# Performance work log

Hardware: AMD Instinct MI355X
Metric: run time of the kernel (lower is better)

The kernel has to match this reference:

```python
import math
import jax, jax.numpy as jnp
import numpy as np

SIN_DIM = 8
HEADS = 4
HID = 64
EMBED = 6 + 1 + 3 * SIN_DIM + 5 + 2  # 38


def _sinusoidal(v):
    # v: [N] -> [N, SIN_DIM], interleaved sin/cos as in torch.stack(...).flatten(-2)
    div = jnp.exp(jnp.arange(0, SIN_DIM, 2, dtype=jnp.float32) * (-math.log(10000.0) / SIN_DIM))
    scaled = v[:, None] * div  # [N, SIN_DIM//2]
    return jnp.stack([jnp.sin(scaled), jnp.cos(scaled)], axis=-1).reshape(v.shape[0], SIN_DIM)


def _feature_embed(x):
    nt = jnp.clip(x[:, 0].astype(jnp.int32), 0, 5)
    role = jnp.clip(x[:, 5].astype(jnp.int32), 0, 4)
    return jnp.concatenate([
        jax.nn.one_hot(nt, 6, dtype=x.dtype),
        jnp.log1p(x[:, 1])[:, None],
        _sinusoidal(x[:, 2]),
        _sinusoidal(x[:, 3]),
        _sinusoidal(x[:, 4] * 100.0),
        jax.nn.one_hot(role, 5, dtype=x.dtype),
        x[:, 6:7],
        x[:, 7:8],
    ], axis=-1)  # [N, 38]


def _gat(x, adj, W, a_src, a_dst, concat):
    N = x.shape[0]
    h = (x @ W).reshape(N, HEADS, HID)                       # [N,H,D]
    src = jnp.einsum('nhd,hd->nh', h, a_src)                 # [N,H]
    dst = jnp.einsum('nhd,hd->nh', h, a_dst)                 # [N,H]
    e = src[:, None, :] + dst[None, :, :]                    # [N,N,H]
    e = jnp.where(e > 0, e, 0.2 * e)                         # leaky_relu(0.2)
    e = jnp.where(adj[:, :, None] > 0, e, -jnp.inf)
    a = jax.nn.softmax(e, axis=1)                            # softmax over neighbors j
    out = jnp.einsum('njh,nhd->nhd'.replace('nj', 'ij').replace('nhd,', 'jhd,').replace('->nhd', '->ihd'), a, h) if False else jnp.einsum('ijh,jhd->ihd', a, h)
    if concat:
        return out.reshape(N, HEADS * HID)
    return out.mean(axis=1)


def _layernorm(x, g, b, eps=1e-5):
    mu = x.mean(axis=-1, keepdims=True)
    var = ((x - mu) ** 2).mean(axis=-1, keepdims=True)
    return (x - mu) / jnp.sqrt(var + eps) * g + b


def setup_inputs() -> dict:
    key = jax.random.key(0)
    ks = jax.random.split(key, 16)
    N, C = 4096, 512
    # raw node features per FeatureEmbedding docstring
    nt = jax.random.randint(ks[0], (N,), 0, 6).astype(jnp.float32)
    arity = jax.random.randint(ks[1], (N,), 0, 5).astype(jnp.float32)
    arg_pos = jax.random.randint(ks[2], (N,), 0, 8).astype(jnp.float32)
    depth = jax.random.randint(ks[3], (N,), 0, 12).astype(jnp.float32)
    age = jax.random.uniform(ks[4], (N,))
    role = jax.random.randint(ks[5], (N,), 0, 5).astype(jnp.float32)
    pol = jax.random.bernoulli(ks[6], 0.5, (N,)).astype(jnp.float32)
    eq = jax.random.bernoulli(ks[7], 0.2, (N,)).astype(jnp.float32)
    node_features = jnp.stack([nt, arity, arg_pos, depth, age, role, pol, eq], axis=-1)
    adj = (jax.random.uniform(ks[8], (N, N)) < 0.01).astype(jnp.float32)
    adj = jnp.maximum(adj, jnp.eye(N, dtype=jnp.float32))  # self-loops
    pm = (jax.random.uniform(ks[9], (C, N)) < (8.0 / N)).astype(jnp.float32)
    pool_matrix = pm / jnp.clip(pm.sum(axis=1, keepdims=True), 1.0, None)
    def xavier(k, shape):
        fan = shape[0] + shape[-1]
        return jax.random.normal(k, shape, dtype=jnp.float32) * math.sqrt(2.0 / fan)
    return {
        'node_features': node_features, 'adj': adj, 'pool_matrix': pool_matrix,
        'W1': xavier(ks[10], (EMBED, HID * HEADS)),
        'a_src1': xavier(ks[11], (HEADS, HID)), 'a_dst1': xavier(ks[12], (HEADS, HID)),
        'g1': jnp.ones((HID * HEADS,), jnp.float32), 'b1': jnp.zeros((HID * HEADS,), jnp.float32),
        'W2': xavier(ks[13], (HID * HEADS, HID * HEADS)),
        'a_src2': xavier(ks[14], (HEADS, HID)), 'a_dst2': xavier(ks[15], (HEADS, HID)),
        'g2': jnp.ones((HID,), jnp.float32), 'b2': jnp.zeros((HID,), jnp.float32),
        'Ws': xavier(jax.random.fold_in(key, 100), (HID, HID)), 'bs': jnp.zeros((HID,), jnp.float32),
        'Wo': xavier(jax.random.fold_in(key, 101), (HID, 1)), 'bo': jnp.zeros((1,), jnp.float32),
    }


def reference(node_features, adj, pool_matrix, W1, a_src1, a_dst1, g1, b1,
              W2, a_src2, a_dst2, g2, b2, Ws, bs, Wo, bo):
    x = _feature_embed(node_features)                         # [N, 38]
    # layer 1: concat heads -> [N, 256]
    x = jax.nn.elu(_layernorm(_gat(x, adj, W1, a_src1, a_dst1, True), g1, b1))
    # layer 2: mean over heads -> [N, 64]  (dropout is eval-mode no-op)
    x = jax.nn.elu(_layernorm(_gat(x, adj, W2, a_src2, a_dst2, False), g2, b2))
    clause_emb = pool_matrix @ x                               # [C, 64]
    h = jax.nn.relu(clause_emb @ Ws + bs)                      # MLP scorer
    return (h @ Wo + bo)[:, 0]                                 # [C]
```

## Files before the change

kernel.cpp:

```cpp
#include <hip/hip_runtime.h>
#include <math.h>

#define N 4096
#define C 512
#define EMB 38
#define HEADS 4
#define HID 64
#define F1 256
#define MAXN 128
#define RPB 8

__device__ __forceinline__ float wr_sum(float v) {
#pragma unroll
    for (int o = 32; o > 0; o >>= 1) v += __shfl_xor(v, o);
    return v;
}
__device__ __forceinline__ float wr_max(float v) {
#pragma unroll
    for (int o = 32; o > 0; o >>= 1) v = fmaxf(v, __shfl_xor(v, o));
    return v;
}

__global__ __launch_bounds__(256) void k_build(const float* __restrict__ adj,
                                               int* __restrict__ cnt, int* __restrict__ idx) {
    int wv = threadIdx.x >> 6, lane = threadIdx.x & 63;
    int i = blockIdx.x * 4 + wv;
    __shared__ int stage[4][MAXN];
    const float4* row = (const float4*)(adj + (size_t)i * N);
    float4 v[16];
#pragma unroll
    for (int it = 0; it < 16; ++it) v[it] = row[it * 64 + lane];
    unsigned long long below = (1ull << lane) - 1;
    int base = 0;
#pragma unroll
    for (int it = 0; it < 16; ++it) {
        int col0 = 4 * (it * 64 + lane);
        float vals[4] = {v[it].x, v[it].y, v[it].z, v[it].w};
#pragma unroll
        for (int comp = 0; comp < 4; ++comp) {
            unsigned long long m = __ballot(vals[comp] > 0.f);
            if (vals[comp] > 0.f) {
                int p = base + __popcll(m & below);
                if (p < MAXN) stage[wv][p] = col0 + comp;
            }
            base += __popcll(m);
        }
    }
    int c = min(base, MAXN);
    __syncthreads();
    if (lane < c)      idx[i * MAXN + lane]      = stage[wv][lane];
    if (lane + 64 < c) idx[i * MAXN + lane + 64] = stage[wv][lane + 64];
    if (lane == 0) cnt[i] = c;
}

__global__ __launch_bounds__(256) void k_gemm1(const float* __restrict__ nf, const float* __restrict__ W1,
                                               const float* __restrict__ asrc, const float* __restrict__ adst,
                                               float* __restrict__ h1, float* __restrict__ s1, float* __restrict__ d1) {
    int n0 = blockIdx.x * RPB, tid = threadIdx.x;
    __shared__ float fs[RPB][8];
    __shared__ float xs[RPB][40];
    if (tid < RPB * 8) fs[tid >> 3][tid & 7] = nf[(size_t)n0 * 8 + tid];
    if (tid < RPB * 2) xs[tid >> 1][38 + (tid & 1)] = 0.f;
    __syncthreads();
    {
        int r = tid & 7;
        int t = tid >> 3;
        const float* f = fs[r];
        for (int pass = 0; pass < 2; ++pass, t += 32) {
            if (t >= EMB) break;
            float val;
            if (t < 6) { int nt = min(max((int)f[0], 0), 5); val = (t == nt) ? 1.f : 0.f; }
            else if (t == 6) val = log1pf(f[1]);
            else if (t < 31) {
                int q = (t - 7) & 7, s = (t - 7) >> 3, m = q >> 1;
                float base = (s == 0) ? f[2] : (s == 1) ? f[3] : f[4] * 100.f;
                float div = expf((2.f * m) * (-logf(10000.f) / 8.f));
                float sc = base * div;
                val = (q & 1) ? cosf(sc) : sinf(sc);
            }
            else if (t < 36) { int role = min(max((int)f[5], 0), 4); val = (t - 31 == role) ? 1.f : 0.f; }
            else val = (t == 36) ? f[6] : f[7];
            xs[r][t] = val;
        }
    }
    __syncthreads();
    float acc[RPB];
#pragma unroll
    for (int r = 0; r < RPB; ++r) acc[r] = 0.f;
#pragma unroll
    for (int kk = 0; kk < 9; ++kk) {
        float w0 = W1[(4 * kk + 0) * F1 + tid];
        float w1 = W1[(4 * kk + 1) * F1 + tid];
        float w2 = W1[(4 * kk + 2) * F1 + tid];
        float w3 = W1[(4 * kk + 3) * F1 + tid];
#pragma unroll
        for (int r = 0; r < RPB; ++r) {
            float4 x = *(const float4*)&xs[r][4 * kk];
            acc[r] = fmaf(x.x, w0, fmaf(x.y, w1, fmaf(x.z, w2, fmaf(x.w, w3, acc[r]))));
        }
    }
#pragma unroll
    for (int k = 36; k < EMB; ++k) {
        float wvv = W1[k * F1 + tid];
#pragma unroll
        for (int r = 0; r < RPB; ++r) acc[r] = fmaf(xs[r][k], wvv, acc[r]);
    }
    int h = tid >> 6, lane = tid & 63;
    float av = asrc[tid], dv = adst[tid];
#pragma unroll
    for (int r = 0; r < RPB; ++r) {
        h1[(size_t)(n0 + r) * F1 + tid] = acc[r];
        float ss = wr_sum(acc[r] * av);
        float dd = wr_sum(acc[r] * dv);
        if (lane == 0) { s1[(n0 + r) * HEADS + h] = ss; d1[(n0 + r) * HEADS + h] = dd; }
    }
}

__global__ __launch_bounds__(256) void k_gemm2(const float* __restrict__ x1, const float* __restrict__ W2,
                                               const float* __restrict__ asrc, const float* __restrict__ adst,
                                               float* __restrict__ h2, float* __restrict__ s2, float* __restrict__ d2) {
    int n0 = blockIdx.x * RPB, tid = threadIdx.x;
    __shared__ float4 xs4[RPB][F1 / 4];
    {
        int r = tid >> 5, kk = tid & 31;
        const float4* x1v = (const float4*)x1;
        xs4[r][kk]      = x1v[(size_t)(n0 + r) * 64 + kk];
        xs4[r][kk + 32] = x1v[(size_t)(n0 + r) * 64 + kk + 32];
    }
    __syncthreads();
    float acc[RPB];
#pragma unroll
    for (int r = 0; r < RPB; ++r) acc[r] = 0.f;
    for (int kk = 0; kk < F1 / 4; ++kk) {
        float w0 = W2[(4 * kk + 0) * F1 + tid];
        float w1 = W2[(4 * kk + 1) * F1 + tid];
        float w2 = W2[(4 * kk + 2) * F1 + tid];
        float w3 = W2[(4 * kk + 3) * F1 + tid];
#pragma unroll
        for (int r = 0; r < RPB; ++r) {
            float4 x = xs4[r][kk];
            acc[r] = fmaf(x.x, w0, fmaf(x.y, w1, fmaf(x.z, w2, fmaf(x.w, w3, acc[r]))));
        }
    }
    int h = tid >> 6, lane = tid & 63;
    float av = asrc[tid], dv = adst[tid];
#pragma unroll
    for (int r = 0; r < RPB; ++r) {
        h2[(size_t)(n0 + r) * F1 + tid] = acc[r];
        float ss = wr_sum(acc[r] * av);
        float dd = wr_sum(acc[r] * dv);
        if (lane == 0) { s2[(n0 + r) * HEADS + h] = ss; d2[(n0 + r) * HEADS + h] = dd; }
    }
}

__global__ __launch_bounds__(256) void k_agg1(const float* __restrict__ h1, const float* __restrict__ s1,
                                              const float* __restrict__ d1, const int* __restrict__ cnt,
                                              const int* __restrict__ idx, const float* __restrict__ g,
                                              const float* __restrict__ b, float* __restrict__ xo) {
    int i = blockIdx.x, tid = threadIdx.x;
    int wv = tid >> 6, lane = tid & 63;
    __shared__ int nbrs[MAXN];
    __shared__ float wts[HEADS][MAXN + 1];
    __shared__ float lsum[HEADS];
    __shared__ float sacc[4][F1];
    __shared__ float red[HEADS];
    int c = cnt[i];
    if (tid < c) nbrs[tid] = idx[i * MAXN + tid];
    __syncthreads();
    if (tid < c) {
        float4 dd = ((const float4*)d1)[nbrs[tid]];
        float4 ss = ((const float4*)s1)[i];
        float e0 = ss.x + dd.x, e1 = ss.y + dd.y, e2 = ss.z + dd.z, e3 = ss.w + dd.w;
        wts[0][tid] = e0 > 0.f ? e0 : 0.2f * e0;
        wts[1][tid] = e1 > 0.f ? e1 : 0.2f * e1;
        wts[2][tid] = e2 > 0.f ? e2 : 0.2f * e2;
        wts[3][tid] = e3 > 0.f ? e3 : 0.2f * e3;
    }
    __syncthreads();
    {
        float m = -INFINITY;
        for (int jj = lane; jj < c; jj += 64) m = fmaxf(m, wts[wv][jj]);
        m = wr_max(m);
        float l = 0.f;
        for (int jj = lane; jj < c; jj += 64) { float t = expf(wts[wv][jj] - m); wts[wv][jj] = t; l += t; }
        l = wr_sum(l);
        if (lane == 0) lsum[wv] = l;
    }
    __syncthreads();
    int hq = lane >> 4;
    const float4* hv = (const float4*)h1;
    float4 acc = {0.f, 0.f, 0.f, 0.f};
    int jj = wv;
    for (; jj + 12 < c; jj += 16) {
        int na = nbrs[jj], nb = nbrs[jj + 4], nc = nbrs[jj + 8], nd = nbrs[jj + 12];
        float wa = wts[hq][jj], wb = wts[hq][jj + 4], wc = wts[hq][jj + 8], wd = wts[hq][jj + 12];
        float4 va = hv[(size_t)na * 64 + lane];
        float4 vb = hv[(size_t)nb * 64 + lane];
        float4 vc = hv[(size_t)nc * 64 + lane];
        float4 vd = hv[(size_t)nd * 64 + lane];
        acc.x = fmaf(wa, va.x, acc.x); acc.y = fmaf(wa, va.y, acc.y);
        acc.z = fmaf(wa, va.z, acc.z); acc.w = fmaf(wa, va.w, acc.w);
        acc.x = fmaf(wb, vb.x, acc.x); acc.y = fmaf(wb, vb.y, acc.y);
        acc.z = fmaf(wb, vb.z, acc.z); acc.w = fmaf(wb, vb.w, acc.w);
        acc.x = fmaf(wc, vc.x, acc.x); acc.y = fmaf(wc, vc.y, acc.y);
        acc.z = fmaf(wc, vc.z, acc.z); acc.w = fmaf(wc, vc.w, acc.w);
        acc.x = fmaf(wd, vd.x, acc.x); acc.y = fmaf(wd, vd.y, acc.y);
        acc.z = fmaf(wd, vd.z, acc.z); acc.w = fmaf(wd, vd.w, acc.w);
    }
    for (; jj < c; jj += 4) {
        int na = nbrs[jj];
        float wa = wts[hq][jj];
        float4 va = hv[(size_t)na * 64 + lane];
        acc.x = fmaf(wa, va.x, acc.x); acc.y = fmaf(wa, va.y, acc.y);
        acc.z = fmaf(wa, va.z, acc.z); acc.w = fmaf(wa, va.w, acc.w);
    }
    ((float4*)&sacc[wv][0])[lane] = acc;
    __syncthreads();
    float tot = (sacc[0][tid] + sacc[1][tid] + sacc[2][tid] + sacc[3][tid]) / lsum[wv];
    float s = wr_sum(tot);
    if (lane == 0) red[wv] = s;
    __syncthreads();
    float mu = (red[0] + red[1] + red[2] + red[3]) * (1.f / F1);
    float dvv = tot - mu;
    float s2 = wr_sum(dvv * dvv);
    __syncthreads();
    if (lane == 0) red[wv] = s2;
    __syncthreads();
    float var = (red[0] + red[1] + red[2] + red[3]) * (1.f / F1);
    float y = dvv * rsqrtf(var + 1e-5f) * g[tid] + b[tid];
    xo[(size_t)i * F1 + tid] = y > 0.f ? y : expm1f(y);
}

__global__ __launch_bounds__(256) void k_agg2(const float* __restrict__ h2, const float* __restrict__ s2,
                                              const float* __restrict__ d2, const int* __restrict__ cnt,
                                              const int* __restrict__ idx, const float* __restrict__ g,
                                              const float* __restrict__ b, float* __restrict__ xo) {
    int i = blockIdx.x, tid = threadIdx.x;
    int wv = tid >> 6, lane = tid & 63;
    __shared__ int nbrs[MAXN];
    __shared__ float wts[HEADS][MAXN + 1];
    __shared__ float lsum[HEADS];
    __shared__ float sacc[4][F1];
    int c = cnt[i];
    if (tid < c) nbrs[tid] = idx[i * MAXN + tid];
    __syncthreads();
    if (tid < c) {
        float4 dd = ((const float4*)d2)[nbrs[tid]];
        float4 ss = ((const float4*)s2)[i];
        float e0 = ss.x + dd.x, e1 = ss.y + dd.y, e2 = ss.z + dd.z, e3 = ss.w + dd.w;
        wts[0][tid] = e0 > 0.f ? e0 : 0.2f * e0;
        wts[1][tid] = e1 > 0.f ? e1 : 0.2f * e1;
        wts[2][tid] = e2 > 0.f ? e2 : 0.2f * e2;
        wts[3][tid] = e3 > 0.f ? e3 : 0.2f * e3;
    }
    __syncthreads();
    {
        float m = -INFINITY;
        for (int jj = lane; jj < c; jj += 64) m = fmaxf(m, wts[wv][jj]);
        m = wr_max(m);
        float l = 0.f;
        for (int jj = lane; jj < c; jj += 64) { float t = expf(wts[wv][jj] - m); wts[wv][jj] = t; l += t; }
        l = wr_sum(l);
        if (lane == 0) lsum[wv] = l;
    }
    __syncthreads();
    int hq = lane >> 4;
    const float4* hvv = (const float4*)h2;
    float4 acc = {0.f, 0.f, 0.f, 0.f};
    int jj = wv;
    for (; jj + 12 < c; jj += 16) {
        int na = nbrs[jj], nb = nbrs[jj + 4], nc = nbrs[jj + 8], nd = nbrs[jj + 12];
        float wa = wts[hq][jj], wb = wts[hq][jj + 4], wc = wts[hq][jj + 8], wd = wts[hq][jj + 12];
        float4 va = hvv[(size_t)na * 64 + lane];
        float4 vb = hvv[(size_t)nb * 64 + lane];
        float4 vc = hvv[(size_t)nc * 64 + lane];
        float4 vd = hvv[(size_t)nd * 64 + lane];
        acc.x = fmaf(wa, va.x, acc.x); acc.y = fmaf(wa, va.y, acc.y);
        acc.z = fmaf(wa, va.z, acc.z); acc.w = fmaf(wa, va.w, acc.w);
        acc.x = fmaf(wb, vb.x, acc.x); acc.y = fmaf(wb, vb.y, acc.y);
        acc.z = fmaf(wb, vb.z, acc.z); acc.w = fmaf(wb, vb.w, acc.w);
        acc.x = fmaf(wc, vc.x, acc.x); acc.y = fmaf(wc, vc.y, acc.y);
        acc.z = fmaf(wc, vc.z, acc.z); acc.w = fmaf(wc, vc.w, acc.w);
        acc.x = fmaf(wd, vd.x, acc.x); acc.y = fmaf(wd, vd.y, acc.y);
        acc.z = fmaf(wd, vd.z, acc.z); acc.w = fmaf(wd, vd.w, acc.w);
    }
    for (; jj < c; jj += 4) {
        int na = nbrs[jj];
        float wa = wts[hq][jj];
        float4 va = hvv[(size_t)na * 64 + lane];
        acc.x = fmaf(wa, va.x, acc.x); acc.y = fmaf(wa, va.y, acc.y);
        acc.z = fmaf(wa, va.z, acc.z); acc.w = fmaf(wa, va.w, acc.w);
    }
    ((float4*)&sacc[wv][0])[lane] = acc;
    __syncthreads();
    if (wv == 0) {
        float t0 = 0.f, t1 = 0.f, t2 = 0.f, t3 = 0.f;
#pragma unroll
        for (int w = 0; w < 4; ++w) {
            t0 += sacc[w][lane];
            t1 += sacc[w][lane + 64];
            t2 += sacc[w][lane + 128];
            t3 += sacc[w][lane + 192];
        }
        float mv = (t0 / lsum[0] + t1 / lsum[1] + t2 / lsum[2] + t3 / lsum[3]) * 0.25f;
        float mu = wr_sum(mv) * (1.f / HID);
        float dvv = mv - mu;
        float var = wr_sum(dvv * dvv) * (1.f / HID);
        float y = dvv * rsqrtf(var + 1e-5f) * g[lane] + b[lane];
        xo[i * HID + lane] = y > 0.f ? y : expm1f(y);
    }
}

__global__ __launch_bounds__(256) void k_poolscore(const float* __restrict__ pm, const float* __restrict__ x2,
                                                   const float* __restrict__ Ws, const float* __restrict__ bs,
                                                   const float* __restrict__ Wo, const float* __restrict__ bo,
                                                   float* __restrict__ out) {
    int c = blockIdx.x, tid = threadIdx.x;
    int w = tid >> 6, lane = tid & 63;
    __shared__ float sacc[4][HID];
    __shared__ float ce_s[HID];
    float acc = 0.f;
    const float4* pmv = (const float4*)(pm + (size_t)c * N);
#pragma unroll
    for (int it = 0; it < 4; ++it) {
        int vi = w * 256 + it * 64 + lane;
        float4 p4 = pmv[vi];
        float pc[4] = {p4.x, p4.y, p4.z, p4.w};
#pragma unroll
        for (int comp = 0; comp < 4; ++comp) {
            unsigned long long msk = __ballot(pc[comp] != 0.f);
            while (msk) {
                int bpos = __ffsll(msk) - 1;
                msk &= msk - 1;
                float pj = __shfl(pc[comp], bpos);
                int j = (w * 256 + it * 64 + bpos) * 4 + comp;
                acc += pj * x2[(size_t)j * HID + lane];
            }
        }
    }
    sacc[w][lane] = acc;
    __syncthreads();
    if (w == 0) ce_s[lane] = sacc[0][lane] + sacc[1][lane] + sacc[2][lane] + sacc[3][lane];
    __syncthreads();
    if (w == 0) {
        float hd = bs[lane];
#pragma unroll 8
        for (int k = 0; k < HID; ++k) hd = fmaf(ce_s[k], Ws[k * HID + lane], hd);
        hd = fmaxf(hd, 0.f);
        float v = wr_sum(hd * Wo[lane]);
        if (lane == 0) out[c] = v + bo[0];
    }
}

extern "C" void kernel_launch(void* const* d_in, const int* in_sizes, int n_in,
                              void* d_out, int out_size, void* d_ws, size_t ws_size,
                              hipStream_t stream) {
    const float* nf  = (const float*)d_in[0];
    const float* adj = (const float*)d_in[1];
    const float* pm  = (const float*)d_in[2];
    const float* W1  = (const float*)d_in[3];
    const float* as1 = (const float*)d_in[4];
    const float* ad1 = (const float*)d_in[5];
    const float* g1  = (const float*)d_in[6];
    const float* b1  = (const float*)d_in[7];
    const float* W2  = (const float*)d_in[8];
    const float* as2 = (const float*)d_in[9];
    const float* ad2 = (const float*)d_in[10];
    const float* g2  = (const float*)d_in[11];
    const float* b2  = (const float*)d_in[12];
    const float* Ws  = (const float*)d_in[13];
    const float* bs  = (const float*)d_in[14];
    const float* Wo  = (const float*)d_in[15];
    const float* bo  = (const float*)d_in[16];
    float* out = (float*)d_out;

    float* p = (float*)d_ws;
    float* h1  = p; p += (size_t)N * F1;
    float* s1  = p; p += (size_t)N * HEADS;
    float* d1  = p; p += (size_t)N * HEADS;
    float* x1  = p; p += (size_t)N * F1;
    float* h2  = p; p += (size_t)N * F1;
    float* s2  = p; p += (size_t)N * HEADS;
    float* d2  = p; p += (size_t)N * HEADS;
    float* x2  = p; p += (size_t)N * HID;
    int* cnt = (int*)p;
    int* idx = cnt + N;

    k_build<<<N / 4, 256, 0, stream>>>(adj, cnt, idx);
    k_gemm1<<<N / RPB, 256, 0, stream>>>(nf, W1, as1, ad1, h1, s1, d1);
    k_agg1<<<N, 256, 0, stream>>>(h1, s1, d1, cnt, idx, g1, b1, x1);
    k_gemm2<<<N / RPB, 256, 0, stream>>>(x1, W2, as2, ad2, h2, s2, d2);
    k_agg2<<<N, 256, 0, stream>>>(h2, s2, d2, cnt, idx, g2, b2, x2);
    k_poolscore<<<C, 256, 0, stream>>>(pm, x2, Ws, bs, Wo, bo, out);
}
```

Before: 196.6 us.

## Fuse adjacency build with layer-1 GEMM and deepen neighbor-gather unrolling

Merges the adjacency-list build and the layer-1 feature GEMM into one launch, interleaving two build blocks with one GEMM block, so a kernel launch is saved and the two independent stages overlap on the device. The neighbor aggregation loops in both attention layers gain an 8-way batched gather to keep more loads in flight. LayerNorm now computes variance as E[x²]−mean² in a single reduction pass, removing one barrier but with somewhat weaker numerical stability. The layer-2 GEMM k-loop also gets an unroll pragma.

```diff
diff --git a/kernel.cpp b/kernel.cpp
--- a/kernel.cpp
+++ b/kernel.cpp
@@ -21,44 +21,50 @@
     return v;
 }
 
-__global__ __launch_bounds__(256) void k_build(const float* __restrict__ adj,
-                                               int* __restrict__ cnt, int* __restrict__ idx) {
-    int wv = threadIdx.x >> 6, lane = threadIdx.x & 63;
-    int i = blockIdx.x * 4 + wv;
+__global__ __launch_bounds__(256) void k_phase1(const float* __restrict__ adj,
+                                                int* __restrict__ cnt, int* __restrict__ idx,
+                                                const float* __restrict__ nf, const float* __restrict__ W1,
+                                                const float* __restrict__ asrc, const float* __restrict__ adst,
+                                                float* __restrict__ h1, float* __restrict__ s1,
+                                                float* __restrict__ d1) {
+    int g = blockIdx.x / 3, r3 = blockIdx.x % 3;
+    int tid = threadIdx.x;
+    int wv = tid >> 6, lane = tid & 63;
     __shared__ int stage[4][MAXN];
-    const float4* row = (const float4*)(adj + (size_t)i * N);
-    float4 v[16];
-#pragma unroll
-    for (int it = 0; it < 16; ++it) v[it] = row[it * 64 + lane];
-    unsigned long long below = (1ull << lane) - 1;
-    int base = 0;
-#pragma unroll
-    for (int it = 0; it < 16; ++it) {
-        int col0 = 4 * (it * 64 + lane);
-        float vals[4] = {v[it].x, v[it].y, v[it].z, v[it].w};
-#pragma unroll
-        for (int comp = 0; comp < 4; ++comp) {
-            unsigned long long m = __ballot(vals[comp] > 0.f);
-            if (vals[comp] > 0.f) {
-                int p = base + __popcll(m & below);
-                if (p < MAXN) stage[wv][p] = col0 + comp;
-            }
-            base += __popcll(m);
-        }
-    }
-    int c = min(base, MAXN);
-    __syncthreads();
-    if (lane < c)      idx[i * MAXN + lane]      = stage[wv][lane];
-    if (lane + 64 < c) idx[i * MAXN + lane + 64] = stage[wv][lane + 64];
-    if (lane == 0) cnt[i] = c;
-}
-
-__global__ __launch_bounds__(256) void k_gemm1(const float* __restrict__ nf, const float* __restrict__ W1,
-                                               const float* __restrict__ asrc, const float* __restrict__ adst,
-                                               float* __restrict__ h1, float* __restrict__ s1, float* __restrict__ d1) {
-    int n0 = blockIdx.x * RPB, tid = threadIdx.x;
     __shared__ float fs[RPB][8];
     __shared__ float xs[RPB][40];
+
+    if (r3 != 2) {
+        int i = (2 * g + r3) * 4 + wv;
+        const float4* row = (const float4*)(adj + (size_t)i * N);
+        float4 v[16];
+#pragma unroll
+        for (int it = 0; it < 16; ++it) v[it] = row[it * 64 + lane];
+        unsigned long long below = (1ull << lane) - 1;
+        int base = 0;
+#pragma unroll
+        for (int it = 0; it < 16; ++it) {
+            int col0 = 4 * (it * 64 + lane);
+            float vals[4] = {v[it].x, v[it].y, v[it].z, v[it].w};
+#pragma unroll
+            for (int comp = 0; comp < 4; ++comp) {
+                unsigned long long m = __ballot(vals[comp] > 0.f);
+                if (vals[comp] > 0.f) {
+                    int p = base + __popcll(m & below);
+                    if (p < MAXN) stage[wv][p] = col0 + comp;
+                }
+                base += __popcll(m);
+            }
+        }
+        int c = min(base, MAXN);
+        __syncthreads();
+        if (lane < c)      idx[i * MAXN + lane]      = stage[wv][lane];
+        if (lane + 64 < c) idx[i * MAXN + lane + 64] = stage[wv][lane + 64];
+        if (lane == 0) cnt[i] = c;
+        return;
+    }
+
+    int n0 = g * RPB;
     if (tid < RPB * 8) fs[tid >> 3][tid & 7] = nf[(size_t)n0 * 8 + tid];
     if (tid < RPB * 2) xs[tid >> 1][38 + (tid & 1)] = 0.f;
     __syncthreads();
@@ -105,15 +111,98 @@
 #pragma unroll
         for (int r = 0; r < RPB; ++r) acc[r] = fmaf(xs[r][k], wvv, acc[r]);
     }
-    int h = tid >> 6, lane = tid & 63;
+    int h = tid >> 6, ln = tid & 63;
     float av = asrc[tid], dv = adst[tid];
 #pragma unroll
     for (int r = 0; r < RPB; ++r) {
         h1[(size_t)(n0 + r) * F1 + tid] = acc[r];
         float ss = wr_sum(acc[r] * av);
         float dd = wr_sum(acc[r] * dv);
-        if (lane == 0) { s1[(n0 + r) * HEADS + h] = ss; d1[(n0 + r) * HEADS + h] = dd; }
-    }
+        if (ln == 0) { s1[(n0 + r) * HEADS + h] = ss; d1[(n0 + r) * HEADS + h] = dd; }
+    }
+}
+
+__global__ __launch_bounds__(256) void k_agg1(const float* __restrict__ h1, const float* __restrict__ s1,
+                                              const float* __restrict__ d1, const int* __restrict__ cnt,
+                                              const int* __restrict__ idx, const float* __restrict__ g,
+                                              const float* __restrict__ b, float* __restrict__ xo) {
+    int i = blockIdx.x, tid = threadIdx.x;
+    int wv = tid >> 6, lane = tid & 63;
+    __shared__ int nbrs[MAXN];
+    __shared__ float wts[HEADS][MAXN + 1];
+    __shared__ float lsum[HEADS];
+    __shared__ float sacc[4][F1];
+    __shared__ float red[HEADS], red2[HEADS];
+    int c = cnt[i];
+    if (tid < c) nbrs[tid] = idx[i * MAXN + tid];
+    __syncthreads();
+    if (tid < c) {
+        float4 dd = ((const float4*)d1)[nbrs[tid]];
+        float4 ss = ((const float4*)s1)[i];
+        float e0 = ss.x + dd.x, e1 = ss.y + dd.y, e2 = ss.z + dd.z, e3 = ss.w + dd.w;
+        wts[0][tid] = e0 > 0.f ? e0 : 0.2f * e0;
+        wts[1][tid] = e1 > 0.f ? e1 : 0.2f * e1;
+        wts[2][tid] = e2 > 0.f ? e2 : 0.2f * e2;
+        wts[3][tid] = e3 > 0.f ? e3 : 0.2f * e3;
+    }
+    __syncthreads();
+    {
+        float m = -INFINITY;
+        for (int jj = lane; jj < c; jj += 64) m = fmaxf(m, wts[wv][jj]);
+        m = wr_max(m);
+        float l = 0.f;
+        for (int jj = lane; jj < c; jj += 64) { float t = expf(wts[wv][jj] - m); wts[wv][jj] = t; l += t; }
+        l = wr_sum(l);
+        if (lane == 0) lsum[wv] = l;
+    }
+    __syncthreads();
+    int hq = lane >> 4;
+    const float4* hv = (const float4*)h1;
+    float4 acc = {0.f, 0.f, 0.f, 0.f};
+    int jj = wv;
+    for (; jj + 28 < c; jj += 32) {
+        int n[8]; float w[8]; float4 v[8];
+#pragma unroll
+        for (int u = 0; u < 8; ++u) { n[u] = nbrs[jj + 4 * u]; w[u] = wts[hq][jj + 4 * u]; }
+#pragma unroll
+        for (int u = 0; u < 8; ++u) v[u] = hv[(size_t)n[u] * 64 + lane];
+#pragma unroll
+        for (int u = 0; u < 8; ++u) {
+            acc.x = fmaf(w[u], v[u].x, acc.x); acc.y = fmaf(w[u], v[u].y, acc.y);
+            acc.z = fmaf(w[u], v[u].z, acc.z); acc.w = fmaf(w[u], v[u].w, acc.w);
+        }
+    }
+    for (; jj + 12 < c; jj += 16) {
+        int n[4]; float w[4]; float4 v[4];
+#pragma unroll
+        for (int u = 0; u < 4; ++u) { n[u] = nbrs[jj + 4 * u]; w[u] = wts[hq][jj + 4 * u]; }
+#pragma unroll
+        for (int u = 0; u < 4; ++u) v[u] = hv[(size_t)n[u] * 64 + lane];
+#pragma unroll
+        for (int u = 0; u < 4; ++u) {
+            acc.x = fmaf(w[u], v[u].x, acc.x); acc.y = fmaf(w[u], v[u].y, acc.y);
+            acc.z = fmaf(w[u], v[u].z, acc.z); acc.w = fmaf(w[u], v[u].w, acc.w);
+        }
+    }
+    for (; jj < c; jj += 4) {
+        int na = nbrs[jj];
+        float wa = wts[hq][jj];
+        float4 va = hv[(size_t)na * 64 + lane];
+        acc.x = fmaf(wa, va.x, acc.x); acc.y = fmaf(wa, va.y, acc.y);
+        acc.z = fmaf(wa, va.z, acc.z); acc.w = fmaf(wa, va.w, acc.w);
+    }
+    ((float4*)&sacc[wv][0])[lane] = acc;
+    __syncthreads();
+    float tot = (sacc[0][tid] + sacc[1][tid] + sacc[2][tid] + sacc[3][tid]) / lsum[wv];
+    float s = wr_sum(tot);
+    float q = wr_sum(tot * tot);
+    if (lane == 0) { red[wv] = s; red2[wv] = q; }
+    __syncthreads();
+    float mu = (red[0] + red[1] + red[2] + red[3]) * (1.f / F1);
+    float ex2 = (red2[0] + red2[1] + red2[2] + red2[3]) * (1.f / F1);
+    float var = ex2 - mu * mu;
+    float y = (tot - mu) * rsqrtf(var + 1e-5f) * g[tid] + b[tid];
+    xo[(size_t)i * F1 + tid] = y > 0.f ? y : expm1f(y);
 }
 
 __global__ __launch_bounds__(256) void k_gemm2(const float* __restrict__ x1, const float* __restrict__ W2,
@@ -131,6 +220,7 @@
     float acc[RPB];
 #pragma unroll
     for (int r = 0; r < RPB; ++r) acc[r] = 0.f;
+#pragma unroll 4
     for (int kk = 0; kk < F1 / 4; ++kk) {
         float w0 = W2[(4 * kk + 0) * F1 + tid];
         float w1 = W2[(4 * kk + 1) * F1 + tid];
@@ -151,84 +241,6 @@
         float dd = wr_sum(acc[r] * dv);
         if (lane == 0) { s2[(n0 + r) * HEADS + h] = ss; d2[(n0 + r) * HEADS + h] = dd; }
     }
-}
-
-__global__ __launch_bounds__(256) void k_agg1(const float* __restrict__ h1, const float* __restrict__ s1,
-                                              const float* __restrict__ d1, const int* __restrict__ cnt,
-                                              const int* __restrict__ idx, const float* __restrict__ g,
-                                              const float* __restrict__ b, float* __restrict__ xo) {
-    int i = blockIdx.x, tid = threadIdx.x;
-    int wv = tid >> 6, lane = tid & 63;
-    __shared__ int nbrs[MAXN];
-    __shared__ float wts[HEADS][MAXN + 1];
-    __shared__ float lsum[HEADS];
-    __shared__ float sacc[4][F1];
-    __shared__ float red[HEADS];
-    int c = cnt[i];
-    if (tid < c) nbrs[tid] = idx[i * MAXN + tid];
-    __syncthreads();
-    if (tid < c) {
-        float4 dd = ((const float4*)d1)[nbrs[tid]];
-        float4 ss = ((const float4*)s1)[i];
-        float e0 = ss.x + dd.x, e1 = ss.y + dd.y, e2 = ss.z + dd.z, e3 = ss.w + dd.w;
-        wts[0][tid] = e0 > 0.f ? e0 : 0.2f * e0;
-        wts[1][tid] = e1 > 0.f ? e1 : 0.2f * e1;
-        wts[2][tid] = e2 > 0.f ? e2 : 0.2f * e2;
-        wts[3][tid] = e3 > 0.f ? e3 : 0.2f * e3;
-    }
-    __syncthreads();
-    {
-        float m = -INFINITY;
-        for (int jj = lane; jj < c; jj += 64) m = fmaxf(m, wts[wv][jj]);
-        m = wr_max(m);
-        float l = 0.f;
-        for (int jj = lane; jj < c; jj += 64) { float t = expf(wts[wv][jj] - m); wts[wv][jj] = t; l += t; }
-        l = wr_sum(l);
-        if (lane == 0) lsum[wv] = l;
-    }
-    __syncthreads();
-    int hq = lane >> 4;
-    const float4* hv = (const float4*)h1;
-    float4 acc = {0.f, 0.f, 0.f, 0.f};
-    int jj = wv;
-    for (; jj + 12 < c; jj += 16) {
-        int na = nbrs[jj], nb = nbrs[jj + 4], nc = nbrs[jj + 8], nd = nbrs[jj + 12];
-        float wa = wts[hq][jj], wb = wts[hq][jj + 4], wc = wts[hq][jj + 8], wd = wts[hq][jj + 12];
-        float4 va = hv[(size_t)na * 64 + lane];
-        float4 vb = hv[(size_t)nb * 64 + lane];
-        float4 vc = hv[(size_t)nc * 64 + lane];
-        float4 vd = hv[(size_t)nd * 64 + lane];
-        acc.x = fmaf(wa, va.x, acc.x); acc.y = fmaf(wa, va.y, acc.y);
-        acc.z = fmaf(wa, va.z, acc.z); acc.w = fmaf(wa, va.w, acc.w);
-        acc.x = fmaf(wb, vb.x, acc.x); acc.y = fmaf(wb, vb.y, acc.y);
-        acc.z = fmaf(wb, vb.z, acc.z); acc.w = fmaf(wb, vb.w, acc.w);
-        acc.x = fmaf(wc, vc.x, acc.x); acc.y = fmaf(wc, vc.y, acc.y);
-        acc.z = fmaf(wc, vc.z, acc.z); acc.w = fmaf(wc, vc.w, acc.w);
-        acc.x = fmaf(wd, vd.x, acc.x); acc.y = fmaf(wd, vd.y, acc.y);
-        acc.z = fmaf(wd, vd.z, acc.z); acc.w = fmaf(wd, vd.w, acc.w);
-    }
-    for (; jj < c; jj += 4) {
-        int na = nbrs[jj];
-        float wa = wts[hq][jj];
-        float4 va = hv[(size_t)na * 64 + lane];
-        acc.x = fmaf(wa, va.x, acc.x); acc.y = fmaf(wa, va.y, acc.y);
-        acc.z = fmaf(wa, va.z, acc.z); acc.w = fmaf(wa, va.w, acc.w);
-    }
-    ((float4*)&sacc[wv][0])[lane] = acc;
-    __syncthreads();
-    float tot = (sacc[0][tid] + sacc[1][tid] + sacc[2][tid] + sacc[3][tid]) / lsum[wv];
-    float s = wr_sum(tot);
-    if (lane == 0) red[wv] = s;
-    __syncthreads();
-    float mu = (red[0] + red[1] + red[2] + red[3]) * (1.f / F1);
-    float dvv = tot - mu;
-    float s2 = wr_sum(dvv * dvv);
-    __syncthreads();
-    if (lane == 0) red[wv] = s2;
-    __syncthreads();
-    float var = (red[0] + red[1] + red[2] + red[3]) * (1.f / F1);
-    float y = dvv * rsqrtf(var + 1e-5f) * g[tid] + b[tid];
-    xo[(size_t)i * F1 + tid] = y > 0.f ? y : expm1f(y);
 }
 
 __global__ __launch_bounds__(256) void k_agg2(const float* __restrict__ h2, const float* __restrict__ s2,
@@ -268,21 +280,29 @@
     const float4* hvv = (const float4*)h2;
     float4 acc = {0.f, 0.f, 0.f, 0.f};
     int jj = wv;
+    for (; jj + 28 < c; jj += 32) {
+        int n[8]; float w[8]; float4 v[8];
+#pragma unroll
+        for (int u = 0; u < 8; ++u) { n[u] = nbrs[jj + 4 * u]; w[u] = wts[hq][jj + 4 * u]; }
+#pragma unroll
+        for (int u = 0; u < 8; ++u) v[u] = hvv[(size_t)n[u] * 64 + lane];
+#pragma unroll
+        for (int u = 0; u < 8; ++u) {
+            acc.x = fmaf(w[u], v[u].x, acc.x); acc.y = fmaf(w[u], v[u].y, acc.y);
+            acc.z = fmaf(w[u], v[u].z, acc.z); acc.w = fmaf(w[u], v[u].w, acc.w);
+        }
+    }
     for (; jj + 12 < c; jj += 16) {
-        int na = nbrs[jj], nb = nbrs[jj + 4], nc = nbrs[jj + 8], nd = nbrs[jj + 12];
-        float wa = wts[hq][jj], wb = wts[hq][jj + 4], wc = wts[hq][jj + 8], wd = wts[hq][jj + 12];
-        float4 va = hvv[(size_t)na * 64 + lane];
-        float4 vb = hvv[(size_t)nb * 64 + lane];
-        float4 vc = hvv[(size_t)nc * 64 + lane];
-        float4 vd = hvv[(size_t)nd * 64 + lane];
-        acc.x = fmaf(wa, va.x, acc.x); acc.y = fmaf(wa, va.y, acc.y);
-        acc.z = fmaf(wa, va.z, acc.z); acc.w = fmaf(wa, va.w, acc.w);
-        acc.x = fmaf(wb, vb.x, acc.x); acc.y = fmaf(wb, vb.y, acc.y);
-        acc.z = fmaf(wb, vb.z, acc.z); acc.w = fmaf(wb, vb.w, acc.w);
-        acc.x = fmaf(wc, vc.x, acc.x); acc.y = fmaf(wc, vc.y, acc.y);
-        acc.z = fmaf(wc, vc.z, acc.z); acc.w = fmaf(wc, vc.w, acc.w);
-        acc.x = fmaf(wd, vd.x, acc.x); acc.y = fmaf(wd, vd.y, acc.y);
-        acc.z = fmaf(wd, vd.z, acc.z); acc.w = fmaf(wd, vd.w, acc.w);
+        int n[4]; float w[4]; float4 v[4];
+#pragma unroll
+        for (int u = 0; u < 4; ++u) { n[u] = nbrs[jj + 4 * u]; w[u] = wts[hq][jj + 4 * u]; }
+#pragma unroll
+        for (int u = 0; u < 4; ++u) v[u] = hvv[(size_t)n[u] * 64 + lane];
+#pragma unroll
+        for (int u = 0; u < 4; ++u) {
+            acc.x = fmaf(w[u], v[u].x, acc.x); acc.y = fmaf(w[u], v[u].y, acc.y);
+            acc.z = fmaf(w[u], v[u].z, acc.z); acc.w = fmaf(w[u], v[u].w, acc.w);
+        }
     }
     for (; jj < c; jj += 4) {
         int na = nbrs[jj];
@@ -304,9 +324,9 @@
         }
         float mv = (t0 / lsum[0] + t1 / lsum[1] + t2 / lsum[2] + t3 / lsum[3]) * 0.25f;
         float mu = wr_sum(mv) * (1.f / HID);
-        float dvv = mv - mu;
-        float var = wr_sum(dvv * dvv) * (1.f / HID);
-        float y = dvv * rsqrtf(var + 1e-5f) * g[lane] + b[lane];
+        float q  = wr_sum(mv * mv) * (1.f / HID);
+        float var = q - mu * mu;
+        float y = (mv - mu) * rsqrtf(var + 1e-5f) * g[lane] + b[lane];
         xo[i * HID + lane] = y > 0.f ? y : expm1f(y);
     }
 }
@@ -386,8 +406,7 @@
     int* cnt = (int*)p;
     int* idx = cnt + N;
 
-    k_build<<<N / 4, 256, 0, stream>>>(adj, cnt, idx);
-    k_gemm1<<<N / RPB, 256, 0, stream>>>(nf, W1, as1, ad1, h1, s1, d1);
+    k_phase1<<<(N / 4) + (N / RPB), 256, 0, stream>>>(adj, cnt, idx, nf, W1, as1, ad1, h1, s1, d1);
     k_agg1<<<N, 256, 0, stream>>>(h1, s1, d1, cnt, idx, g1, b1, x1);
     k_gemm2<<<N / RPB, 256, 0, stream>>>(x1, W2, as2, ad2, h2, s2, d2);
     k_agg2<<<N, 256, 0, stream>>>(h2, s2, d2, cnt, idx, g2, b2, x2);
```

Result: slower. 210.4 us (+7.0%).
